# Kernel optimization log

Hardware: AMD Instinct MI355X
Metric: run time of the kernel (lower is better)

Reference implementation:

```python
import jax, jax.numpy as jnp
import numpy as np

EMB = 1024
HID = 2048
NH = 16
NKV = 16
NE = 8
TOPK = 2
WIN = 2048
B = 2
L = 2048
HD = EMB // NH  # 64


def _layer_norm(x, g, b, eps=1e-5):
    m = jnp.mean(x, axis=-1, keepdims=True)
    v = jnp.mean((x - m) ** 2, axis=-1, keepdims=True)
    return (x - m) / jnp.sqrt(v + eps) * g + b


def setup_inputs() -> dict:
    key = jax.random.key(0)
    ks = jax.random.split(key, 12)
    w = lambda k, shape: (jax.random.normal(k, shape, jnp.float32) * 0.02)
    return {
        "x": jax.random.normal(ks[0], (B, L, EMB), jnp.float32),
        "position_idx": 0,
        "ln1_g": jnp.ones((EMB,), jnp.float32),
        "ln1_b": jnp.zeros((EMB,), jnp.float32),
        "ln2_g": jnp.ones((EMB,), jnp.float32),
        "ln2_b": jnp.zeros((EMB,), jnp.float32),
        "Wq": w(ks[1], (EMB, EMB)),
        "Wk": w(ks[2], (EMB, EMB)),
        "Wv": w(ks[3], (EMB, EMB)),
        "Wo": w(ks[4], (EMB, EMB)),
        "Wr": w(ks[5], (EMB, NE)),
        "W1": w(ks[6], (NE, EMB, HID)),
        "b1": jnp.zeros((NE, HID), jnp.float32),
        "W2": w(ks[7], (NE, HID, EMB)),
        "b2": jnp.zeros((NE, EMB), jnp.float32),
    }


def reference(x, position_idx, ln1_g, ln1_b, ln2_g, ln2_b, Wq, Wk, Wv, Wo, Wr, W1, b1, W2, b2):
    Bn, Ln, D = x.shape
    scale = 1.0 / (HD ** 0.5)

    # --- sliding-window attention (cache=None path) ---
    h = _layer_norm(x, ln1_g, ln1_b)
    q = (h @ Wq).reshape(Bn, Ln, NH, HD).transpose(0, 2, 1, 3)   # [B,H,L,hd]
    k = (h @ Wk).reshape(Bn, Ln, NKV, HD).transpose(0, 2, 1, 3)  # [B,KV,L,hd]
    v = (h @ Wv).reshape(Bn, Ln, NKV, HD).transpose(0, 2, 1, 3)
    k = k[:, :, -WIN:]
    v = v[:, :, -WIN:]
    qpk = NH // NKV
    if qpk > 1:
        k = jnp.repeat(k, qpk, axis=1)
        v = jnp.repeat(v, qpk, axis=1)
    scores = jnp.einsum('bhqd,bhkd->bhqk', q, k) * scale
    S = k.shape[2]
    i = jnp.arange(Ln)[:, None]
    j = jnp.arange(S)[None, :]
    mask = (j > i) | (j < i + position_idx - WIN)  # causal + sliding window
    scores = jnp.where(mask[None, None], -jnp.inf, scores)
    attn = jax.nn.softmax(scores, axis=-1)
    attn_out = jnp.einsum('bhqk,bhkd->bqhd', attn, v).reshape(Bn, Ln, D) @ Wo
    x = x + attn_out

    # --- top-k MoE ---
    h2 = _layer_norm(x, ln2_g, ln2_b)
    logits = h2 @ Wr                               # [B,L,E]
    top_v, top_i = jax.lax.top_k(logits, TOPK)     # [B,L,K]
    top_w = jax.nn.softmax(top_v, axis=-1)
    out = jnp.zeros_like(x)
    for e in range(NE):
        # combine weight for expert e per token (sums over top-k slots)
        we = jnp.sum(jnp.where(top_i == e, top_w, 0.0), axis=-1)  # [B,L]
        he = jax.nn.silu(h2 @ W1[e] + b1[e])
        out = out + we[..., None] * (he @ W2[e] + b2[e])
    return x + out
```

## Files before the change

### kernel.cpp

```cpp
#include <hip/hip_runtime.h>
#include <hip/hip_bf16.h>

typedef __hip_bfloat16 bf16;
typedef __attribute__((ext_vector_type(8))) short bf16x8;
typedef __attribute__((ext_vector_type(4))) float f32x4;

constexpr int kEMB = 1024;
constexpr int kHID = 2048;
constexpr int kNH  = 16;
constexpr int kNE  = 8;
constexpr int kL   = 2048;
constexpr int kHD  = 64;
constexpr int kT   = 4096;
constexpr int kSLOTS = kT * 2;
constexpr int kWIN = 2048;

__device__ __forceinline__ unsigned short f2bfbits(float f){
  bf16 h = __float2bfloat16(f);
  return __builtin_bit_cast(unsigned short, h);
}
__device__ __forceinline__ float bfbits2f(unsigned short u){
  unsigned int x = ((unsigned int)u) << 16;
  return __builtin_bit_cast(float, x);
}
__device__ __forceinline__ void gld_lds16(const void* g, void* s){
  __builtin_amdgcn_global_load_lds((const __attribute__((address_space(1))) void*)g,
                                   (__attribute__((address_space(3))) void*)s, 16, 0, 0);
}

__global__ __launch_bounds__(256) void tconv_k(const float* __restrict__ src, bf16* __restrict__ dst,
                                               int R, int C){
  __shared__ float tile[32][33];
  const int tx = threadIdx.x & 31, ty = threadIdx.x >> 5;
  const int bx = blockIdx.x * 32, by = blockIdx.y * 32;
  const size_t base = (size_t)blockIdx.z * R * C;
  #pragma unroll
  for (int i = 0; i < 32; i += 8)
    tile[ty + i][tx] = src[base + (size_t)(by + ty + i) * C + bx + tx];
  __syncthreads();
  #pragma unroll
  for (int i = 0; i < 32; i += 8)
    dst[base + (size_t)(bx + ty + i) * R + by + tx] = __float2bfloat16(tile[tx][ty + i]);
}

__global__ __launch_bounds__(256) void vtrans_k(const bf16* __restrict__ v, bf16* __restrict__ vt){
  __shared__ unsigned short tile[32][33];
  const int tx = threadIdx.x & 31, ty = threadIdx.x >> 5;
  const int l0 = blockIdx.x * 32, d0 = blockIdx.y * 32;
  const unsigned short* src = (const unsigned short*)v + (size_t)blockIdx.z * kL * kHD;
  unsigned short* dst = (unsigned short*)vt + (size_t)blockIdx.z * kHD * kL;
  #pragma unroll
  for (int i = 0; i < 32; i += 8)
    tile[ty + i][tx] = src[(size_t)(l0 + ty + i) * kHD + d0 + tx];
  __syncthreads();
  #pragma unroll
  for (int i = 0; i < 32; i += 8)
    dst[(size_t)(d0 + ty + i) * kL + l0 + tx] = tile[tx][ty + i];
}

__device__ __forceinline__ float block_sum(float v, float* red){
  #pragma unroll
  for (int x = 32; x > 0; x >>= 1) v += __shfl_xor(v, x, 64);
  const int lane = threadIdx.x & 63, w = threadIdx.x >> 6;
  if (lane == 0) red[w] = v;
  __syncthreads();
  float s = red[0] + red[1] + red[2] + red[3];
  __syncthreads();
  return s;
}

__global__ __launch_bounds__(256) void ln_k(
    const float* __restrict__ x, const float* __restrict__ g, const float* __restrict__ bta,
    bf16* __restrict__ h)
{
  __shared__ float red[4];
  const int row = blockIdx.x, tid = threadIdx.x;
  const float4 v = ((const float4*)(x + (size_t)row * kEMB))[tid];
  float s = block_sum(v.x + v.y + v.z + v.w, red);
  const float mean = s * (1.0f / kEMB);
  const float dx = v.x - mean, dy = v.y - mean, dz = v.z - mean, dw = v.w - mean;
  float ss = block_sum(dx*dx + dy*dy + dz*dz + dw*dw, red);
  const float rstd = rsqrtf(ss * (1.0f / kEMB) + 1e-5f);
  const float4 gg = ((const float4*)g)[tid];
  const float4 bb = ((const float4*)bta)[tid];
  ushort4 pk;
  pk.x = f2bfbits(dx * rstd * gg.x + bb.x);
  pk.y = f2bfbits(dy * rstd * gg.y + bb.y);
  pk.z = f2bfbits(dz * rstd * gg.z + bb.z);
  pk.w = f2bfbits(dw * rstd * gg.w + bb.w);
  *(ushort4*)((unsigned short*)h + (size_t)row * kEMB + tid * 4) = pk;
}

__global__ __launch_bounds__(256) void ln2_k(
    const float* __restrict__ x, const float* __restrict__ P,
    const float* __restrict__ g, const float* __restrict__ bta,
    float* __restrict__ out, bf16* __restrict__ h, const float* __restrict__ Wr,
    int* __restrict__ top_i, float* __restrict__ top_w)
{
  __shared__ float red[4];
  __shared__ float red8[4][8];
  const int row = blockIdx.x, tid = threadIdx.x;
  const float4 vx = ((const float4*)(x + (size_t)row * kEMB))[tid];
  const float4 p0 = ((const float4*)(P + (size_t)row * kEMB))[tid];
  const float4 p1 = ((const float4*)(P + (size_t)(kT + row) * kEMB))[tid];
  float4 v;
  v.x = vx.x + p0.x + p1.x; v.y = vx.y + p0.y + p1.y;
  v.z = vx.z + p0.z + p1.z; v.w = vx.w + p0.w + p1.w;
  ((float4*)(out + (size_t)row * kEMB))[tid] = v;
  float s = block_sum(v.x + v.y + v.z + v.w, red);
  const float mean = s * (1.0f / kEMB);
  const float dx = v.x - mean, dy = v.y - mean, dz = v.z - mean, dw = v.w - mean;
  float ss = block_sum(dx*dx + dy*dy + dz*dz + dw*dw, red);
  const float rstd = rsqrtf(ss * (1.0f / kEMB) + 1e-5f);
  const float4 gg = ((const float4*)g)[tid];
  const float4 bb = ((const float4*)bta)[tid];
  const float n0 = dx * rstd * gg.x + bb.x;
  const float n1 = dy * rstd * gg.y + bb.y;
  const float n2 = dz * rstd * gg.z + bb.z;
  const float n3 = dw * rstd * gg.w + bb.w;
  ushort4 pk;
  pk.x = f2bfbits(n0); pk.y = f2bfbits(n1); pk.z = f2bfbits(n2); pk.w = f2bfbits(n3);
  *(ushort4*)((unsigned short*)h + (size_t)row * kEMB + tid * 4) = pk;
  float part[8];
  #pragma unroll
  for (int e = 0; e < 8; e++) part[e] = 0.f;
  const float* wrp = Wr + (size_t)tid * 4 * kNE;
  const float nv[4] = {n0, n1, n2, n3};
  #pragma unroll
  for (int i = 0; i < 4; i++)
    #pragma unroll
    for (int e = 0; e < 8; e++) part[e] += nv[i] * wrp[i * kNE + e];
  #pragma unroll
  for (int xm = 32; xm > 0; xm >>= 1)
    #pragma unroll
    for (int e = 0; e < 8; e++) part[e] += __shfl_xor(part[e], xm, 64);
  const int lane = tid & 63, w = tid >> 6;
  if (lane == 0)
    #pragma unroll
    for (int e = 0; e < 8; e++) red8[w][e] = part[e];
  __syncthreads();
  if (tid == 0){
    float lg[8];
    #pragma unroll
    for (int e = 0; e < 8; e++) lg[e] = red8[0][e] + red8[1][e] + red8[2][e] + red8[3][e];
    int i0 = 0; float v0 = lg[0];
    #pragma unroll
    for (int e = 1; e < 8; e++) if (lg[e] > v0){ v0 = lg[e]; i0 = e; }
    int i1 = -1; float v1 = -3.4e38f;
    #pragma unroll
    for (int e = 0; e < 8; e++) if (e != i0 && lg[e] > v1){ v1 = lg[e]; i1 = e; }
    const float w0 = 1.0f / (1.0f + __expf(v1 - v0));
    top_i[row * 2] = i0; top_i[row * 2 + 1] = i1;
    top_w[row * 2] = w0; top_w[row * 2 + 1] = 1.0f - w0;
  }
}

template<int MODE>
__global__ __launch_bounds__(256) void gemm_k(
    const bf16* __restrict__ A, const bf16* __restrict__ BT, int K,
    float* __restrict__ fdst, bf16* __restrict__ bdst,
    const float* __restrict__ bias,
    const float* __restrict__ roww, const int* __restrict__ rowtok,
    const int* __restrict__ offs)
{
  __shared__ alignas(16) unsigned short As[2][128 * 64];
  __shared__ alignas(16) unsigned short Bs[2][128 * 64];
  const int tid = threadIdx.x, lane = tid & 63, w = tid >> 6;
  const int wr = w >> 1, wc = w & 1;
  int e = 0, rbase = 0, rend = 0, bx, by;
  if (MODE == 2){
    e = blockIdx.x & 7; const int s = blockIdx.x >> 3; by = s >> 4; bx = s & 15;
    rbase = offs[e]; rend = offs[e + 1];
    if (by * 128 >= rend - rbase) return;
  } else if (MODE == 3){
    e = blockIdx.x & 7; const int s = blockIdx.x >> 3; by = s >> 3; bx = s & 7;
    rbase = offs[e]; rend = offs[e + 1];
    if (by * 128 >= rend - rbase) return;
  } else {
    bx = blockIdx.x; by = blockIdx.y;
  }
  int kt0 = 0, nkt = K / 64;
  if (MODE == 1){ kt0 = blockIdx.z * (K / 2); nkt = K / 128; }
  const int m0 = by * 128, n0 = bx * 128;
  const bf16* Bp = BT;
  const float* biasp = bias;
  if (MODE == 2){ Bp += (size_t)e * kHID * kEMB; biasp += e * kHID; }
  if (MODE == 3){ Bp += (size_t)e * kEMB * kHID; biasp += e * kEMB; }
  f32x4 acc[4][4] = {};
  const int srow = lane >> 3;
  const int skk  = (lane & 7) * 8;

  size_t aoff[4];
  #pragma unroll
  for (int j = 0; j < 4; j++){
    const int r = w * 32 + j * 8 + srow;
    size_t row;
    if (MODE == 2){ int p = rbase + m0 + r; if (p >= rend) p = rbase; row = (size_t)rowtok[p]; }
    else if (MODE == 3){ int p = rbase + m0 + r; if (p >= rend) p = rbase; row = (size_t)p; }
    else row = (size_t)(m0 + r);
    aoff[j] = row * (size_t)K;
  }

  auto stage = [&](int t, int buf){
    const int kt = kt0 + t * 64;
    #pragma unroll
    for (int j = 0; j < 4; j++){
      const int rr = w * 32 + j * 8;
      gld_lds16(A + aoff[j] + kt + skk, &As[buf][rr * 64]);
      gld_lds16(Bp + (size_t)(n0 + rr + srow) * K + kt + skk, &Bs[buf][rr * 64]);
    }
  };

  stage(0, 0);
  __syncthreads();
  for (int t = 0; t < nkt; t++){
    const int cur = t & 1;
    if (t + 1 < nkt) stage(t + 1, cur ^ 1);
    #pragma unroll
    for (int ks = 0; ks < 2; ks++){
      bf16x8 af[4], bfm[4];
      #pragma unroll
      for (int i = 0; i < 4; i++){
        af[i]  = *(const bf16x8*)&As[cur][(wr * 64 + i * 16 + (lane & 15)) * 64 + ks * 32 + (lane >> 4) * 8];
        bfm[i] = *(const bf16x8*)&Bs[cur][(wc * 64 + i * 16 + (lane & 15)) * 64 + ks * 32 + (lane >> 4) * 8];
      }
      #pragma unroll
      for (int i = 0; i < 4; i++)
        #pragma unroll
        for (int j = 0; j < 4; j++)
          acc[i][j] = __builtin_amdgcn_mfma_f32_16x16x32_bf16(af[i], bfm[j], acc[i][j], 0, 0, 0);
    }
    __syncthreads();
  }

  #pragma unroll
  for (int i = 0; i < 4; i++){
    #pragma unroll
    for (int r = 0; r < 4; r++){
      const int gm = m0 + wr * 64 + i * 16 + (lane >> 4) * 4 + r;
      if (MODE == 1){
        float* pdst = fdst + (size_t)blockIdx.z * kT * kEMB;
        #pragma unroll
        for (int jn = 0; jn < 4; jn++){
          const int gn = n0 + wc * 64 + jn * 16 + (lane & 15);
          pdst[(size_t)gm * kEMB + gn] = acc[i][jn][r];
        }
      } else if (MODE == 2){
        const int p = rbase + gm;
        if (p < rend){
          #pragma unroll
          for (int jn = 0; jn < 4; jn++){
            const int gn = n0 + wc * 64 + jn * 16 + (lane & 15);
            const float vv = acc[i][jn][r] + biasp[gn];
            bdst[(size_t)p * kHID + gn] = __float2bfloat16(vv / (1.0f + __expf(-vv)));
          }
        }
      } else if (MODE == 3){
        const int p = rbase + gm;
        if (p < rend){
          const float wgt = roww[p];
          #pragma unroll
          for (int jn = 0; jn < 4; jn++){
            const int gn = n0 + wc * 64 + jn * 16 + (lane & 15);
            bdst[(size_t)p * kEMB + gn] = __float2bfloat16((acc[i][jn][r] + biasp[gn]) * wgt);
          }
        }
      } else {
        const int bidx = gm >> 11, l = gm & (kL - 1);
        #pragma unroll
        for (int jn = 0; jn < 4; jn++){
          const int gn = n0 + wc * 64 + jn * 16 + (lane & 15);
          const int sec = gn >> 10;
          const int nn = gn & 1023;
          const int hh = nn >> 6, d = nn & 63;
          const float val = acc[i][jn][r] * (sec == 0 ? 0.125f : 1.0f);
          bdst[(size_t)sec * kT * kEMB + (((size_t)bidx * kNH + hh) * kL + l) * kHD + d] =
              __float2bfloat16(val);
        }
      }
    }
  }
}

__global__ __launch_bounds__(256) void attn_k(
    const bf16* __restrict__ q, const bf16* __restrict__ k, const bf16* __restrict__ vt,
    bf16* __restrict__ o, const int* __restrict__ pos)
{
  const int bid = blockIdx.x;
  const int qt = 31 - (bid >> 5);
  const int bh = bid & 31;
  const int tid = threadIdx.x, lane = tid & 63, w = tid >> 6;
  const unsigned short* qp  = (const unsigned short*)q  + (size_t)bh * kL * kHD;
  const unsigned short* kp  = (const unsigned short*)k  + (size_t)bh * kL * kHD;
  const unsigned short* vtp = (const unsigned short*)vt + (size_t)bh * kHD * kL;
  __shared__ alignas(16) unsigned short Ks[2][64 * 64];
  __shared__ alignas(16) unsigned short Vt[2][64 * 64];
  __shared__ alignas(16) unsigned short pl[4 * 16 * 72];
  const int q0 = qt * 64 + w * 16;
  const int pos0 = pos[0];
  const int wlo = pos0 - kWIN;

  bf16x8 qf[2];
  {
    const int qrow = q0 + (lane & 15);
    #pragma unroll
    for (int ks = 0; ks < 2; ks++)
      qf[ks] = *(const bf16x8*)&qp[(size_t)qrow * kHD + ks * 32 + (lane >> 4) * 8];
  }
  float m_run[4], l_run[4];
  f32x4 oacc[4] = {};
  #pragma unroll
  for (int r = 0; r < 4; r++){ m_run[r] = -1e30f; l_run[r] = 0.f; }

  auto stage = [&](int kt, int buf){
    #pragma unroll
    for (int j = 0; j < 2; j++){
      const int r = w * 16 + j * 8 + (lane >> 3);
      const int c = (lane & 7) ^ (r & 7);
      gld_lds16(kp  + (size_t)(kt * 64 + r) * 64 + c * 8, &Ks[buf][(w * 16 + j * 8) * 64]);
      gld_lds16(vtp + (size_t)r * kL + kt * 64 + c * 8,   &Vt[buf][(w * 16 + j * 8) * 64]);
    }
  };

  stage(0, 0);
  for (int kt = 0; kt <= qt; kt++){
    const int buf = kt & 1;
    __syncthreads();
    if (kt < qt) stage(kt + 1, buf ^ 1);

    f32x4 s[4];
    #pragma unroll
    for (int kbk = 0; kbk < 4; kbk++){
      const int row = kbk * 16 + (lane & 15);
      f32x4 a = {0.f, 0.f, 0.f, 0.f};
      #pragma unroll
      for (int ks = 0; ks < 2; ks++){
        const int chnk = ks * 4 + (lane >> 4);
        const bf16x8 kf = *(const bf16x8*)&Ks[buf][row * 64 + ((chnk ^ (row & 7)) * 8)];
        a = __builtin_amdgcn_mfma_f32_16x16x32_bf16(qf[ks], kf, a, 0, 0, 0);
      }
      s[kbk] = a;
    }
    const bool needmask = (kt == qt) || (kt * 64 < q0 + 16 + wlo);
    if (needmask){
      #pragma unroll
      for (int kbk = 0; kbk < 4; kbk++){
        const int j = kt * 64 + kbk * 16 + (lane & 15);
        #pragma unroll
        for (int r = 0; r < 4; r++){
          const int i = q0 + (lane >> 4) * 4 + r;
          if (j > i || j < i + wlo) s[kbk][r] = -1e30f;
        }
      }
    }
    float tm[4];
    #pragma unroll
    for (int r = 0; r < 4; r++) tm[r] = -1e30f;
    #pragma unroll
    for (int kbk = 0; kbk < 4; kbk++)
      #pragma unroll
      for (int r = 0; r < 4; r++) tm[r] = fmaxf(tm[r], s[kbk][r]);
    #pragma unroll
    for (int xm = 1; xm < 16; xm <<= 1)
      #pragma unroll
      for (int r = 0; r < 4; r++) tm[r] = fmaxf(tm[r], __shfl_xor(tm[r], xm, 64));
    bool need = false;
    #pragma unroll
    for (int r = 0; r < 4; r++) need |= (tm[r] > m_run[r] + 8.0f);
    if (__any(need)){
      #pragma unroll
      for (int r = 0; r < 4; r++){
        const float mn = fmaxf(m_run[r], tm[r]);
        const float corr = __expf(m_run[r] - mn);
        m_run[r] = mn;
        l_run[r] *= corr;
        #pragma unroll
        for (int db = 0; db < 4; db++) oacc[db][r] *= corr;
      }
    }
    float ts[4] = {0.f, 0.f, 0.f, 0.f};
    #pragma unroll
    for (int kbk = 0; kbk < 4; kbk++)
      #pragma unroll
      for (int r = 0; r < 4; r++){
        const float p = __expf(s[kbk][r] - m_run[r]);
        s[kbk][r] = p;
        ts[r] += p;
      }
    #pragma unroll
    for (int xm = 1; xm < 16; xm <<= 1)
      #pragma unroll
      for (int r = 0; r < 4; r++) ts[r] += __shfl_xor(ts[r], xm, 64);
    #pragma unroll
    for (int r = 0; r < 4; r++) l_run[r] += ts[r];
    #pragma unroll
    for (int kbk = 0; kbk < 4; kbk++)
      #pragma unroll
      for (int r = 0; r < 4; r++)
        pl[(w * 16 + (lane >> 4) * 4 + r) * 72 + kbk * 16 + (lane & 15)] = f2bfbits(s[kbk][r]);
    asm volatile("s_waitcnt lgkmcnt(0)" ::: "memory");
    __builtin_amdgcn_sched_barrier(0);
    bf16x8 pa[2];
    #pragma unroll
    for (int ks = 0; ks < 2; ks++)
      pa[ks] = *(const bf16x8*)&pl[(w * 16 + (lane & 15)) * 72 + ks * 32 + (lane >> 4) * 8];
    #pragma unroll
    for (int db = 0; db < 4; db++){
      const int row = db * 16 + (lane & 15);
      #pragma unroll
      for (int ks = 0; ks < 2; ks++){
        const int chnk = ks * 4 + (lane >> 4);
        const bf16x8 vf = *(const bf16x8*)&Vt[buf][row * 64 + ((chnk ^ (row & 7)) * 8)];
        oacc[db] = __builtin_amdgcn_mfma_f32_16x16x32_bf16(pa[ks], vf, oacc[db], 0, 0, 0);
      }
    }
  }
  const int hh = bh & (kNH - 1), bidx = bh >> 4;
  #pragma unroll
  for (int db = 0; db < 4; db++){
    #pragma unroll
    for (int r = 0; r < 4; r++){
      const int i = q0 + (lane >> 4) * 4 + r;
      const int d = db * 16 + (lane & 15);
      o[((size_t)(bidx * kL + i)) * kEMB + hh * kHD + d] = __float2bfloat16(oacc[db][r] / l_run[r]);
    }
  }
}

__global__ void zero_k(int* counts){ if (threadIdx.x < kNE) counts[threadIdx.x] = 0; }

__global__ __launch_bounds__(256) void count_k(const int* __restrict__ top_i, int* __restrict__ counts){
  const int idx = blockIdx.x * 256 + threadIdx.x;
  if (idx < kSLOTS) atomicAdd(&counts[top_i[idx]], 1);
}

__global__ void scan_k(const int* __restrict__ counts, int* __restrict__ offs, int* __restrict__ cursor){
  int o = 0;
  for (int e = 0; e < kNE; e++){ offs[e] = o; cursor[e] = o; o += counts[e]; }
  offs[kNE] = o;
}

__global__ __launch_bounds__(256) void assign_k(const int* __restrict__ top_i, const float* __restrict__ top_w,
                                                int* __restrict__ cursor, int* __restrict__ rowtok,
                                                float* __restrict__ roww, int* __restrict__ tok2row){
  const int idx = blockIdx.x * 256 + threadIdx.x;
  if (idx < kSLOTS){
    const int e = top_i[idx];
    const int p = atomicAdd(&cursor[e], 1);
    rowtok[p] = idx >> 1;
    roww[p] = top_w[idx];
    tok2row[idx] = p;
  }
}

__global__ __launch_bounds__(256) void combine_k(float* __restrict__ out, const bf16* __restrict__ g2,
                                                 const int* __restrict__ tok2row){
  const int t = blockIdx.x, c = threadIdx.x * 4;
  const int r0 = tok2row[t * 2], r1 = tok2row[t * 2 + 1];
  const ushort4 ua = *(const ushort4*)((const unsigned short*)g2 + (size_t)r0 * kEMB + c);
  const ushort4 ub = *(const ushort4*)((const unsigned short*)g2 + (size_t)r1 * kEMB + c);
  float* op = out + (size_t)t * kEMB + c;
  float4 ov = *(float4*)op;
  ov.x += bfbits2f(ua.x) + bfbits2f(ub.x);
  ov.y += bfbits2f(ua.y) + bfbits2f(ub.y);
  ov.z += bfbits2f(ua.z) + bfbits2f(ub.z);
  ov.w += bfbits2f(ua.w) + bfbits2f(ub.w);
  *(float4*)op = ov;
}

extern "C" void kernel_launch(void* const* d_in, const int* in_sizes, int n_in,
                              void* d_out, int out_size, void* d_ws, size_t ws_size,
                              hipStream_t stream)
{
  const float* x    = (const float*)d_in[0];
  const int*   pos  = (const int*)d_in[1];
  const float* ln1g = (const float*)d_in[2];
  const float* ln1b = (const float*)d_in[3];
  const float* ln2g = (const float*)d_in[4];
  const float* ln2b = (const float*)d_in[5];
  const float* Wq   = (const float*)d_in[6];
  const float* Wk   = (const float*)d_in[7];
  const float* Wv   = (const float*)d_in[8];
  const float* Wo   = (const float*)d_in[9];
  const float* Wr   = (const float*)d_in[10];
  const float* W1   = (const float*)d_in[11];
  const float* b1   = (const float*)d_in[12];
  const float* W2   = (const float*)d_in[13];
  const float* b2   = (const float*)d_in[14];
  float* out = (float*)d_out;

  char* p = (char*)d_ws;
  auto alloc = [&](size_t bytes) -> char* {
    char* r = p; p += (bytes + 255) & ~(size_t)255; return r;
  };
  bf16* WqkvT = (bf16*)alloc((size_t)3 * kEMB * kEMB * 2);
  bf16* WoT   = (bf16*)alloc((size_t)kEMB * kEMB * 2);
  bf16* W1T   = (bf16*)alloc((size_t)kNE * kEMB * kHID * 2);
  bf16* W2T   = (bf16*)alloc((size_t)kNE * kEMB * kHID * 2);
  bf16* hbf   = (bf16*)alloc((size_t)kT * kEMB * 2);
  bf16* qkv   = (bf16*)alloc((size_t)3 * kT * kEMB * 2);
  bf16* vtbf  = (bf16*)alloc((size_t)kT * kEMB * 2);
  bf16* abf   = (bf16*)alloc((size_t)kT * kEMB * 2);
  bf16* h2bf  = (bf16*)alloc((size_t)kT * kEMB * 2);
  bf16* hebf  = (bf16*)alloc((size_t)kSLOTS * kHID * 2);
  bf16* g2bf  = (bf16*)alloc((size_t)kSLOTS * kEMB * 2);
  int*   top_i   = (int*)alloc(kSLOTS * 4);
  float* top_w   = (float*)alloc(kSLOTS * 4);
  int*   counts  = (int*)alloc(64);
  int*   offs    = (int*)alloc(64);
  int*   cursor  = (int*)alloc(64);
  int*   rowtok  = (int*)alloc(kSLOTS * 4);
  float* rowwgt  = (float*)alloc(kSLOTS * 4);
  int*   tok2row = (int*)alloc(kSLOTS * 4);
  bf16* qbf = qkv;
  bf16* kbf = qkv + (size_t)kT * kEMB;
  bf16* vbf = qkv + (size_t)2 * kT * kEMB;
  float* Pws = (float*)hbf;
  (void)in_sizes; (void)n_in; (void)out_size; (void)ws_size;

  tconv_k<<<dim3(32, 32, 1), 256, 0, stream>>>(Wq, WqkvT, kEMB, kEMB);
  tconv_k<<<dim3(32, 32, 1), 256, 0, stream>>>(Wk, WqkvT + (size_t)kEMB * kEMB, kEMB, kEMB);
  tconv_k<<<dim3(32, 32, 1), 256, 0, stream>>>(Wv, WqkvT + (size_t)2 * kEMB * kEMB, kEMB, kEMB);
  tconv_k<<<dim3(32, 32, 1), 256, 0, stream>>>(Wo, WoT, kEMB, kEMB);
  tconv_k<<<dim3(64, 32, kNE), 256, 0, stream>>>(W1, W1T, kEMB, kHID);
  tconv_k<<<dim3(32, 64, kNE), 256, 0, stream>>>(W2, W2T, kHID, kEMB);

  ln_k<<<kT, 256, 0, stream>>>(x, ln1g, ln1b, hbf);

  gemm_k<4><<<dim3(24, 32), 256, 0, stream>>>(hbf, WqkvT, kEMB, nullptr, qkv, nullptr, nullptr, nullptr, nullptr);

  vtrans_k<<<dim3(kL / 32, kHD / 32, 32), 256, 0, stream>>>(vbf, vtbf);

  attn_k<<<dim3(1024), 256, 0, stream>>>(qbf, kbf, vtbf, abf, pos);

  gemm_k<1><<<dim3(8, 32, 2), 256, 0, stream>>>(abf, WoT, kEMB, Pws, nullptr, nullptr, nullptr, nullptr, nullptr);

  ln2_k<<<kT, 256, 0, stream>>>(x, Pws, ln2g, ln2b, out, h2bf, Wr, top_i, top_w);

  zero_k<<<1, 64, 0, stream>>>(counts);
  count_k<<<kSLOTS / 256, 256, 0, stream>>>(top_i, counts);
  scan_k<<<1, 1, 0, stream>>>(counts, offs, cursor);
  assign_k<<<kSLOTS / 256, 256, 0, stream>>>(top_i, top_w, cursor, rowtok, rowwgt, tok2row);

  gemm_k<2><<<dim3(8 * 32 * 16), 256, 0, stream>>>(h2bf, W1T, kEMB, nullptr, hebf, b1, nullptr, rowtok, offs);
  gemm_k<3><<<dim3(8 * 32 * 8), 256, 0, stream>>>(hebf, W2T, kHID, nullptr, g2bf, b2, rowwgt, nullptr, offs);

  combine_k<<<kT, 256, 0, stream>>>(out, g2bf, tok2row);
}
```

Measured before the change: 414.8 us.

## Add 256x256-tile 8-wave grouped GEMM kernel for MoE expert matmuls

The two MoE expert GEMMs move from the generic 128x128 kernel to a new 512-thread kernel with 256x256 output tiles. It uses XOR-swizzled LDS layouts to avoid bank conflicts, and splits each k-step into four phases that interleave the next tile's loads with MFMA work. Manual vmcnt waits, barriers and setprio control the overlap. Larger tiles raise arithmetic intensity and reuse of expert weights, but experts with few routed tokens waste more of each tile, and the 128 KB of LDS per block limits occupancy.

```diff
diff --git a/kernel.cpp b/kernel.cpp
--- a/kernel.cpp
+++ b/kernel.cpp
@@ -158,56 +158,27 @@
 template<int MODE>
 __global__ __launch_bounds__(256) void gemm_k(
     const bf16* __restrict__ A, const bf16* __restrict__ BT, int K,
-    float* __restrict__ fdst, bf16* __restrict__ bdst,
-    const float* __restrict__ bias,
-    const float* __restrict__ roww, const int* __restrict__ rowtok,
-    const int* __restrict__ offs)
+    float* __restrict__ fdst, bf16* __restrict__ bdst)
 {
   __shared__ alignas(16) unsigned short As[2][128 * 64];
   __shared__ alignas(16) unsigned short Bs[2][128 * 64];
   const int tid = threadIdx.x, lane = tid & 63, w = tid >> 6;
   const int wr = w >> 1, wc = w & 1;
-  int e = 0, rbase = 0, rend = 0, bx, by;
-  if (MODE == 2){
-    e = blockIdx.x & 7; const int s = blockIdx.x >> 3; by = s >> 4; bx = s & 15;
-    rbase = offs[e]; rend = offs[e + 1];
-    if (by * 128 >= rend - rbase) return;
-  } else if (MODE == 3){
-    e = blockIdx.x & 7; const int s = blockIdx.x >> 3; by = s >> 3; bx = s & 7;
-    rbase = offs[e]; rend = offs[e + 1];
-    if (by * 128 >= rend - rbase) return;
-  } else {
-    bx = blockIdx.x; by = blockIdx.y;
-  }
+  const int bx = blockIdx.x, by = blockIdx.y;
   int kt0 = 0, nkt = K / 64;
   if (MODE == 1){ kt0 = blockIdx.z * (K / 2); nkt = K / 128; }
   const int m0 = by * 128, n0 = bx * 128;
-  const bf16* Bp = BT;
-  const float* biasp = bias;
-  if (MODE == 2){ Bp += (size_t)e * kHID * kEMB; biasp += e * kHID; }
-  if (MODE == 3){ Bp += (size_t)e * kEMB * kHID; biasp += e * kEMB; }
   f32x4 acc[4][4] = {};
   const int srow = lane >> 3;
   const int skk  = (lane & 7) * 8;
 
-  size_t aoff[4];
-  #pragma unroll
-  for (int j = 0; j < 4; j++){
-    const int r = w * 32 + j * 8 + srow;
-    size_t row;
-    if (MODE == 2){ int p = rbase + m0 + r; if (p >= rend) p = rbase; row = (size_t)rowtok[p]; }
-    else if (MODE == 3){ int p = rbase + m0 + r; if (p >= rend) p = rbase; row = (size_t)p; }
-    else row = (size_t)(m0 + r);
-    aoff[j] = row * (size_t)K;
-  }
-
   auto stage = [&](int t, int buf){
     const int kt = kt0 + t * 64;
     #pragma unroll
     for (int j = 0; j < 4; j++){
       const int rr = w * 32 + j * 8;
-      gld_lds16(A + aoff[j] + kt + skk, &As[buf][rr * 64]);
-      gld_lds16(Bp + (size_t)(n0 + rr + srow) * K + kt + skk, &Bs[buf][rr * 64]);
+      gld_lds16(A + (size_t)(m0 + rr + srow) * K + kt + skk, &As[buf][rr * 64]);
+      gld_lds16(BT + (size_t)(n0 + rr + srow) * K + kt + skk, &Bs[buf][rr * 64]);
     }
   };
 
@@ -244,26 +215,6 @@
         for (int jn = 0; jn < 4; jn++){
           const int gn = n0 + wc * 64 + jn * 16 + (lane & 15);
           pdst[(size_t)gm * kEMB + gn] = acc[i][jn][r];
-        }
-      } else if (MODE == 2){
-        const int p = rbase + gm;
-        if (p < rend){
-          #pragma unroll
-          for (int jn = 0; jn < 4; jn++){
-            const int gn = n0 + wc * 64 + jn * 16 + (lane & 15);
-            const float vv = acc[i][jn][r] + biasp[gn];
-            bdst[(size_t)p * kHID + gn] = __float2bfloat16(vv / (1.0f + __expf(-vv)));
-          }
-        }
-      } else if (MODE == 3){
-        const int p = rbase + gm;
-        if (p < rend){
-          const float wgt = roww[p];
-          #pragma unroll
-          for (int jn = 0; jn < 4; jn++){
-            const int gn = n0 + wc * 64 + jn * 16 + (lane & 15);
-            bdst[(size_t)p * kEMB + gn] = __float2bfloat16((acc[i][jn][r] + biasp[gn]) * wgt);
-          }
         }
       } else {
         const int bidx = gm >> 11, l = gm & (kL - 1);
@@ -276,6 +227,125 @@
           const float val = acc[i][jn][r] * (sec == 0 ? 0.125f : 1.0f);
           bdst[(size_t)sec * kT * kEMB + (((size_t)bidx * kNH + hh) * kL + l) * kHD + d] =
               __float2bfloat16(val);
+        }
+      }
+    }
+  }
+}
+
+template<int MODE>
+__global__ __launch_bounds__(512, 2) void gemm8_k(
+    const bf16* __restrict__ A, const bf16* __restrict__ BT, int K,
+    bf16* __restrict__ bdst, const float* __restrict__ bias,
+    const float* __restrict__ roww, const int* __restrict__ rowtok,
+    const int* __restrict__ offs)
+{
+  __shared__ alignas(16) unsigned short As[2][2][128 * 64];
+  __shared__ alignas(16) unsigned short Bs[2][2][128 * 64];
+  const int tid = threadIdx.x, lane = tid & 63, w = tid >> 6;
+  const int wr = w >> 2, wc = w & 3;
+  const int e = blockIdx.x & 7, s = blockIdx.x >> 3;
+  const int bx = (MODE == 2) ? (s & 7) : (s & 3);
+  const int by = (MODE == 2) ? (s >> 3) : (s >> 2);
+  const int rbase = offs[e], rend = offs[e + 1];
+  if (by * 256 >= rend - rbase) return;
+  const int m0 = by * 256, n0 = bx * 256;
+  const int NB = (MODE == 2) ? kHID : kEMB;
+  const bf16* Bp = BT + (size_t)e * NB * K;
+  const float* biasp = bias + e * NB;
+  const int nkt = K / 64;
+
+  f32x4 acc[8][4] = {};
+  const int sr  = tid >> 3;
+  const int skk = (((tid & 7) ^ (sr & 7))) * 8;
+
+  int aoff[2][2], boff[2][2];
+  #pragma unroll
+  for (int h = 0; h < 2; h++)
+    #pragma unroll
+    for (int j = 0; j < 2; j++){
+      int p = rbase + m0 + h * 128 + sr + j * 64;
+      if (p >= rend) p = rbase;
+      aoff[h][j] = ((MODE == 2) ? rowtok[p] : p) * K;
+      boff[h][j] = (n0 + h * 128 + sr + j * 64) * K;
+    }
+
+  auto stageA = [&](int t, int h){
+    const int kt = t * 64;
+    gld_lds16(A + aoff[h][0] + kt + skk, &As[t & 1][h][tid * 8]);
+    gld_lds16(A + aoff[h][1] + kt + skk, &As[t & 1][h][(tid + 512) * 8]);
+  };
+  auto stageB = [&](int t, int h){
+    const int kt = t * 64;
+    gld_lds16(Bp + boff[h][0] + kt + skk, &Bs[t & 1][h][tid * 8]);
+    gld_lds16(Bp + boff[h][1] + kt + skk, &Bs[t & 1][h][(tid + 512) * 8]);
+  };
+
+  auto phase = [&](int d, int ks, int mg){
+    bf16x8 af[4], bfr[4];
+    const int c8 = ks * 4 + (lane >> 4);
+    #pragma unroll
+    for (int i = 0; i < 4; i++){
+      const int ar = (mg * 4 + i) * 16 + (lane & 15);
+      af[i] = *(const bf16x8*)&As[d][wr][ar * 64 + (c8 ^ (ar & 7)) * 8];
+    }
+    #pragma unroll
+    for (int j = 0; j < 4; j++){
+      const int br = (wc & 1) * 64 + j * 16 + (lane & 15);
+      bfr[j] = *(const bf16x8*)&Bs[d][wc >> 1][br * 64 + (c8 ^ (br & 7)) * 8];
+    }
+    __builtin_amdgcn_s_setprio(1);
+    #pragma unroll
+    for (int i = 0; i < 4; i++)
+      #pragma unroll
+      for (int j = 0; j < 4; j++)
+        acc[mg * 4 + i][j] = __builtin_amdgcn_mfma_f32_16x16x32_bf16(af[i], bfr[j], acc[mg * 4 + i][j], 0, 0, 0);
+    __builtin_amdgcn_s_setprio(0);
+  };
+
+  stageA(0, 0); stageA(0, 1); stageB(0, 0); stageB(0, 1);
+  asm volatile("s_waitcnt vmcnt(0)" ::: "memory");
+  __builtin_amdgcn_s_barrier();
+
+  for (int t = 0; t < nkt; t++){
+    const int d = t & 1;
+    const bool pre = (t + 1 < nkt);
+    if (pre){ stageA(t + 1, 0); asm volatile("s_waitcnt vmcnt(2)" ::: "memory"); }
+    else    {                    asm volatile("s_waitcnt vmcnt(0)" ::: "memory"); }
+    __builtin_amdgcn_s_barrier();
+    phase(d, 0, 0);
+    __builtin_amdgcn_s_barrier();
+    if (pre) stageA(t + 1, 1);
+    phase(d, 0, 1);
+    __builtin_amdgcn_s_barrier();
+    if (pre) stageB(t + 1, 0);
+    phase(d, 1, 0);
+    __builtin_amdgcn_s_barrier();
+    if (pre) stageB(t + 1, 1);
+    phase(d, 1, 1);
+    __builtin_amdgcn_s_barrier();
+  }
+
+  #pragma unroll
+  for (int mi = 0; mi < 8; mi++){
+    #pragma unroll
+    for (int ri = 0; ri < 4; ri++){
+      const int p = rbase + m0 + wr * 128 + mi * 16 + (lane >> 4) * 4 + ri;
+      if (p < rend){
+        if (MODE == 2){
+          #pragma unroll
+          for (int nj = 0; nj < 4; nj++){
+            const int gn = n0 + wc * 64 + nj * 16 + (lane & 15);
+            const float vv = acc[mi][nj][ri] + biasp[gn];
+            bdst[(size_t)p * NB + gn] = __float2bfloat16(vv / (1.0f + __expf(-vv)));
+          }
+        } else {
+          const float wgt = roww[p];
+          #pragma unroll
+          for (int nj = 0; nj < 4; nj++){
+            const int gn = n0 + wc * 64 + nj * 16 + (lane & 15);
+            bdst[(size_t)p * NB + gn] = __float2bfloat16((acc[mi][nj][ri] + biasp[gn]) * wgt);
+          }
         }
       }
     }
@@ -527,13 +597,13 @@
 
   ln_k<<<kT, 256, 0, stream>>>(x, ln1g, ln1b, hbf);
 
-  gemm_k<4><<<dim3(24, 32), 256, 0, stream>>>(hbf, WqkvT, kEMB, nullptr, qkv, nullptr, nullptr, nullptr, nullptr);
+  gemm_k<4><<<dim3(24, 32), 256, 0, stream>>>(hbf, WqkvT, kEMB, nullptr, qkv);
 
   vtrans_k<<<dim3(kL / 32, kHD / 32, 32), 256, 0, stream>>>(vbf, vtbf);
 
   attn_k<<<dim3(1024), 256, 0, stream>>>(qbf, kbf, vtbf, abf, pos);
 
-  gemm_k<1><<<dim3(8, 32, 2), 256, 0, stream>>>(abf, WoT, kEMB, Pws, nullptr, nullptr, nullptr, nullptr, nullptr);
+  gemm_k<1><<<dim3(8, 32, 2), 256, 0, stream>>>(abf, WoT, kEMB, Pws, nullptr);
 
   ln2_k<<<kT, 256, 0, stream>>>(x, Pws, ln2g, ln2b, out, h2bf, Wr, top_i, top_w);
 
@@ -542,8 +612,8 @@
   scan_k<<<1, 1, 0, stream>>>(counts, offs, cursor);
   assign_k<<<kSLOTS / 256, 256, 0, stream>>>(top_i, top_w, cursor, rowtok, rowwgt, tok2row);
 
-  gemm_k<2><<<dim3(8 * 32 * 16), 256, 0, stream>>>(h2bf, W1T, kEMB, nullptr, hebf, b1, nullptr, rowtok, offs);
-  gemm_k<3><<<dim3(8 * 32 * 8), 256, 0, stream>>>(hebf, W2T, kHID, nullptr, g2bf, b2, rowwgt, nullptr, offs);
+  gemm8_k<2><<<dim3(8 * 8 * 16), 512, 0, stream>>>(h2bf, W1T, kEMB, hebf, b1, nullptr, rowtok, offs);
+  gemm8_k<3><<<dim3(8 * 4 * 16), 512, 0, stream>>>(hebf, W2T, kHID, g2bf, b2, rowwgt, nullptr, offs);
 
   combine_k<<<kT, 256, 0, stream>>>(out, g2bf, tok2row);
 }
```

Measured after the change: 487.1 us. 17.4% more time.
